# Performance work log

Hardware: AMD Instinct MI355X
Metric: run time of the kernel (lower is better)

## Reference

```python
import jax, jax.numpy as jnp
import numpy as np

N_NODES = 20000
N_EDGES = 50000
IN_DIM = 128
HID = 128
OUT_DIM = 64
N_PAIRS = 128
N_LAYERS = 2
N_HEADS = 4


def setup_inputs() -> dict:
    key = jax.random.key(0)
    ks = jax.random.split(key, 32)
    s = 0.05
    def p(k, shape):
        return jax.random.normal(k, shape, jnp.float32) * s
    inp = {}
    inp["node_features"] = jax.random.normal(ks[0], (N_NODES, IN_DIM), jnp.float32)
    inp["edge_index"] = jax.random.randint(ks[1], (2, N_EDGES), 0, N_NODES, jnp.int32)
    inp["edge_timestamps"] = jax.random.uniform(ks[2], (N_EDGES,), jnp.float32)
    inp["target_pairs"] = jax.random.randint(ks[3], (N_PAIRS, 2), 0, N_NODES, jnp.int32)
    inp["in_W"] = p(ks[4], (HID, IN_DIM)); inp["in_b"] = p(ks[5], (HID,))
    inp["te_W1"] = p(ks[6], (N_LAYERS, HID, 1)); inp["te_b1"] = p(ks[7], (N_LAYERS, HID))
    inp["te_W2"] = p(ks[8], (N_LAYERS, HID, HID)); inp["te_b2"] = p(ks[9], (N_LAYERS, HID))
    inp["attn_in_W"] = p(ks[10], (N_LAYERS, 3 * HID, HID)); inp["attn_in_b"] = p(ks[11], (N_LAYERS, 3 * HID))
    inp["attn_out_W"] = p(ks[12], (N_LAYERS, HID, HID)); inp["attn_out_b"] = p(ks[13], (N_LAYERS, HID))
    inp["ft_W"] = p(ks[14], (N_LAYERS, HID, HID)); inp["ft_b"] = p(ks[15], (N_LAYERS, HID))
    inp["op_W"] = p(ks[16], (N_LAYERS, HID, HID)); inp["op_b"] = p(ks[17], (N_LAYERS, HID))
    inp["out1_W"] = p(ks[18], (HID, HID)); inp["out1_b"] = p(ks[19], (HID,))
    inp["out2_W"] = p(ks[20], (OUT_DIM, HID)); inp["out2_b"] = p(ks[21], (OUT_DIM,))
    inp["lp1_W"] = p(ks[22], (HID, 2 * OUT_DIM)); inp["lp1_b"] = p(ks[23], (HID,))
    inp["lp2_W"] = p(ks[24], (HID // 2, HID)); inp["lp2_b"] = p(ks[25], (HID // 2,))
    inp["lp3_W"] = p(ks[26], (1, HID // 2)); inp["lp3_b"] = p(ks[27], (1,))
    return inp


def _forward(node_features, edge_index, edge_timestamps, target_pairs,
             in_W, in_b, te_W1, te_b1, te_W2, te_b2,
             attn_in_W, attn_in_b, attn_out_W, attn_out_b,
             ft_W, ft_b, op_W, op_b,
             out1_W, out1_b, out2_W, out2_b,
             lp1_W, lp1_b, lp2_W, lp2_b, lp3_W, lp3_b):
    N = node_features.shape[0]
    h = in_W.shape[0]
    H = N_HEADS
    d = h // H
    scale = 1.0 / np.sqrt(d).astype(np.float32)
    src, dst = edge_index[0], edge_index[1]
    # flattened target nodes; duplicates compute identical rows so dedup (torch.unique) is unneeded
    targets = target_pairs.reshape(-1)  # [U]
    U = targets.shape[0]
    E = src.shape[0]

    x = node_features @ in_W.T + in_b  # [N, h]
    for l in range(te_W1.shape[0]):
        tf = x @ ft_W[l].T + ft_b[l]                                           # [N, h]
        tfeat = jax.nn.relu(edge_timestamps[:, None] @ te_W1[l].T + te_b1[l])
        tfeat = tfeat @ te_W2[l].T + te_b2[l]                                  # [E, h]
        Wq, Wk, Wv = jnp.split(attn_in_W[l], 3, axis=0)
        bq, bk, bv = jnp.split(attn_in_b[l], 3)
        q = (tf[targets] @ Wq.T + bq).reshape(U, H, d)
        # keys/values are linear in (tf[nbr] + tfeat): split into node term A and edge term B
        Ak = (tf @ Wk.T).reshape(N, H, d)
        Bk = (tfeat @ Wk.T + bk).reshape(E, H, d)
        Av = (tf @ Wv.T).reshape(N, H, d)
        Bv = (tfeat @ Wv.T + bv).reshape(E, H, d)
        is_src = src[None, :] == targets[:, None]          # [U, E]
        mask = is_src | (dst[None, :] == targets[:, None])  # edge incident to target
        nbr = jnp.where(is_src, dst[None, :], src[None, :])  # other endpoint, [U, E]
        qAk = jnp.einsum('uhd,nhd->uhn', q, Ak) * scale      # [U, H, N]
        idx = jnp.broadcast_to(nbr[:, None, :], (U, H, E))
        s_node = jnp.take_along_axis(qAk, idx, axis=2)        # [U, H, E]
        s_edge = jnp.einsum('uhd,ehd->uhe', q, Bk) * scale
        scores = jnp.where(mask[:, None, :], s_node + s_edge, -1e30)
        p = jax.nn.softmax(scores, axis=-1)
        p = jnp.where(mask[:, None, :], p, 0.0)               # [U, H, E]
        out_edge = jnp.einsum('uhe,ehd->uhd', p, Bv)
        # sum_e p * Av[nbr] via per-target scatter of probs into node space
        w = jax.vmap(lambda pe, ne: jax.ops.segment_sum(pe, ne, num_segments=N))(
            p.transpose(0, 2, 1), nbr)                        # [U, N, H]
        out_node = jnp.einsum('unh,nhd->uhd', w, Av)
        attn = (out_node + out_edge).reshape(U, h) @ attn_out_W[l].T + attn_out_b[l]
        has_nbr = mask.any(axis=1)
        agg_in = jnp.where(has_nbr[:, None], attn, tf[targets])
        agg = agg_in @ op_W[l].T + op_b[l]
        x = x.at[targets].set(agg)
        x = jax.nn.relu(x)
    emb = jax.nn.relu(x @ out1_W.T + out1_b) @ out2_W.T + out2_b  # [N, out]
    pair = jnp.concatenate([emb[target_pairs[:, 0]], emb[target_pairs[:, 1]]], axis=1)
    z = jax.nn.relu(pair @ lp1_W.T + lp1_b)
    z = jax.nn.relu(z @ lp2_W.T + lp2_b)
    return jax.nn.sigmoid(z @ lp3_W.T + lp3_b)  # [B, 1]


def reference(node_features, edge_index, edge_timestamps, target_pairs,
              in_W, in_b, te_W1, te_b1, te_W2, te_b2,
              attn_in_W, attn_in_b, attn_out_W, attn_out_b,
              ft_W, ft_b, op_W, op_b,
              out1_W, out1_b, out2_W, out2_b,
              lp1_W, lp1_b, lp2_W, lp2_b, lp3_W, lp3_b):
    return _forward(node_features, edge_index, edge_timestamps, target_pairs,
                    in_W, in_b, te_W1, te_b1, te_W2, te_b2,
                    attn_in_W, attn_in_b, attn_out_W, attn_out_b,
                    ft_W, ft_b, op_W, op_b,
                    out1_W, out1_b, out2_W, out2_b,
                    lp1_W, lp1_b, lp2_W, lp2_b, lp3_W, lp3_b)
```

## Files before the change

kernel.cpp:

```cpp
#include <hip/hip_runtime.h>
#include <math.h>

#define N_NODES 20000
#define N_EDGES 50000
#define N_SLOTS 256
#define N_PAIRS 128
#define CAP 32
#define MSTRIDE 16384
#define NMAT 19
#define TFLAG (1 << 30)
#define HSZ 1024
#define NBLK 256
#define BATCH 16

__device__ __forceinline__ float4 relu4(float4 v) {
    return make_float4(fmaxf(v.x, 0.f), fmaxf(v.y, 0.f), fmaxf(v.z, 0.f), fmaxf(v.w, 0.f));
}
__device__ __forceinline__ float4 add4(float4 a, float4 b) {
    return make_float4(a.x + b.x, a.y + b.y, a.z + b.z, a.w + b.w);
}
__device__ __forceinline__ void fma4(float4& acc, const float4 w, const float s) {
    acc.x = fmaf(w.x, s, acc.x); acc.y = fmaf(w.y, s, acc.y);
    acc.z = fmaf(w.z, s, acc.z); acc.w = fmaf(w.w, s, acc.w);
}
#define F4Z make_float4(0.f, 0.f, 0.f, 0.f)

__device__ __forceinline__ void gbar(unsigned* cnt, unsigned target, bool wait) {
    __syncthreads();
    if (threadIdx.x == 0) {
        __builtin_amdgcn_fence(__ATOMIC_RELEASE, "agent");
        __hip_atomic_fetch_add(cnt, 1u, __ATOMIC_RELAXED, __HIP_MEMORY_SCOPE_AGENT);
        if (wait) {
            int it = 0;
            while (true) {
                unsigned v;
                if ((it++ & 7) != 7)
                    v = __hip_atomic_load(cnt, __ATOMIC_RELAXED,
                                          __HIP_MEMORY_SCOPE_SYSTEM);
                else
                    v = __hip_atomic_fetch_add(cnt, 0u, __ATOMIC_RELAXED,
                                               __HIP_MEMORY_SCOPE_AGENT);
                if (v >= target) break;
                __builtin_amdgcn_s_sleep(16);
            }
            __builtin_amdgcn_fence(__ATOMIC_ACQUIRE, "agent");
        }
    }
    __syncthreads();
}

__device__ __forceinline__ float4 mv_ks1_g8(const float* __restrict__ WT,
                                            const float* __restrict__ xv128,
                                            int g, int jj) {
    const float4* W4 = (const float4*)WT;
    const float4* x4 = (const float4*)xv128;
    float4 acc = F4Z;
#pragma unroll
    for (int kk4 = 0; kk4 < 4; ++kk4) {
        int k4 = g * 4 + kk4;
        float4 xv = x4[k4];
        fma4(acc, W4[(k4 * 4 + 0) * 32 + jj], xv.x);
        fma4(acc, W4[(k4 * 4 + 1) * 32 + jj], xv.y);
        fma4(acc, W4[(k4 * 4 + 2) * 32 + jj], xv.z);
        fma4(acc, W4[(k4 * 4 + 3) * 32 + jj], xv.w);
    }
    return acc;
}
__device__ __forceinline__ float4 mv_ks1_g8_64(const float* __restrict__ WT,
                                               const float* __restrict__ xv128,
                                               int g, int jj) {
    const float4* W4 = (const float4*)WT;
    const float4* x4 = (const float4*)xv128;
    int j16 = jj & 15;
    float4 acc = F4Z;
#pragma unroll
    for (int kk4 = 0; kk4 < 4; ++kk4) {
        int k4 = g * 4 + kk4;
        float4 xv = x4[k4];
        fma4(acc, W4[(k4 * 4 + 0) * 16 + j16], xv.x);
        fma4(acc, W4[(k4 * 4 + 1) * 16 + j16], xv.y);
        fma4(acc, W4[(k4 * 4 + 2) * 16 + j16], xv.z);
        fma4(acc, W4[(k4 * 4 + 3) * 16 + j16], xv.w);
    }
    return acc;
}
__device__ __forceinline__ float4 comb1_g8(const float4* pb, int jj) {
    float4 s = pb[jj];
#pragma unroll
    for (int gp = 1; gp < 8; ++gp) s = add4(s, pb[gp * 32 + jj]);
    return s;
}

__device__ __forceinline__ void mv16_g8(const float* __restrict__ WT,
                                        const float* __restrict__ xs,
                                        int g, int jj, float4* acc) {
    const float4* W4 = (const float4*)WT;
    const float4* x4 = (const float4*)xs;
#pragma unroll
    for (int kk4 = 0; kk4 < 4; ++kk4) {
        int k4 = g * 4 + kk4;
        float4 w0 = W4[(k4 * 4 + 0) * 32 + jj];
        float4 w1 = W4[(k4 * 4 + 1) * 32 + jj];
        float4 w2 = W4[(k4 * 4 + 2) * 32 + jj];
        float4 w3 = W4[(k4 * 4 + 3) * 32 + jj];
#pragma unroll
        for (int e = 0; e < 16; ++e) {
            float4 xv = x4[e * 32 + k4];
            fma4(acc[e], w0, xv.x); fma4(acc[e], w1, xv.y);
            fma4(acc[e], w2, xv.z); fma4(acc[e], w3, xv.w);
        }
    }
}
__device__ __forceinline__ float4 comb16_g8(const float4* pb, int it, int jj) {
    float4 s = pb[it * 32 + jj];
#pragma unroll
    for (int gp = 1; gp < 8; ++gp) s = add4(s, pb[(gp * 16 + it) * 32 + jj]);
    return s;
}

__device__ __forceinline__ float4 mv_ks1(const float* __restrict__ WT,
                                         const float* __restrict__ xv128,
                                         int g, int jj) {
    const float4* W4 = (const float4*)WT;
    const float4* x4 = (const float4*)xv128;
    float4 acc = F4Z;
#pragma unroll 2
    for (int kk4 = 0; kk4 < 8; ++kk4) {
        int k4 = g * 8 + kk4;
        float4 xv = x4[k4];
        fma4(acc, W4[(k4 * 4 + 0) * 32 + jj], xv.x);
        fma4(acc, W4[(k4 * 4 + 1) * 32 + jj], xv.y);
        fma4(acc, W4[(k4 * 4 + 2) * 32 + jj], xv.z);
        fma4(acc, W4[(k4 * 4 + 3) * 32 + jj], xv.w);
    }
    return acc;
}
__device__ __forceinline__ float4 mv_ks1_64(const float* __restrict__ WT,
                                            const float* __restrict__ xv128,
                                            int g, int jj) {
    const float4* W4 = (const float4*)WT;
    const float4* x4 = (const float4*)xv128;
    int j16 = jj & 15;
    float4 acc = F4Z;
#pragma unroll 2
    for (int kk4 = 0; kk4 < 8; ++kk4) {
        int k4 = g * 8 + kk4;
        float4 xv = x4[k4];
        fma4(acc, W4[(k4 * 4 + 0) * 16 + j16], xv.x);
        fma4(acc, W4[(k4 * 4 + 1) * 16 + j16], xv.y);
        fma4(acc, W4[(k4 * 4 + 2) * 16 + j16], xv.z);
        fma4(acc, W4[(k4 * 4 + 3) * 16 + j16], xv.w);
    }
    return acc;
}
__device__ __forceinline__ float4 comb1(const float4* pb, int jj) {
    return add4(add4(pb[jj], pb[32 + jj]), add4(pb[64 + jj], pb[96 + jj]));
}

__device__ __forceinline__ unsigned thash(int key) {
    return ((unsigned)key * 2654435761u) >> 22;
}
__device__ __forceinline__ bool hexists(const int* __restrict__ hkey, int key) {
    unsigned h = thash(key);
    while (true) {
        int k = hkey[h];
        if (k == -1) return false;
        if (k == key) return true;
        h = (h + 1) & (HSZ - 1);
    }
}
__device__ __forceinline__ void hemit_g(const int* __restrict__ hkey,
                                        const int* __restrict__ hval,
                                        int* __restrict__ gcnt,
                                        int2* __restrict__ lst,
                                        int key, int e, int nbrf) {
    unsigned h = thash(key);
    while (true) {
        int k = hkey[h];
        if (k == -1) return;
        if (k == key) {
            int s = hval[h];
            int pos = atomicAdd(&gcnt[s], 1);
            if (pos < CAP) lst[s * CAP + pos] = make_int2(e, nbrf);
        }
        h = (h + 1) & (HSZ - 1);
    }
}

struct Params {
    const float* nf; const int* ei; const float* ts; const int* tp;
    const float* inW; const float* inb;
    const float* teW1; const float* teb1; const float* teW2; const float* teb2;
    const float* aiW; const float* aib; const float* aoW; const float* aob;
    const float* ftW; const float* ftb; const float* opW; const float* opb;
    const float* o1W; const float* o1b; const float* o2W; const float* o2b;
    const float* l1W; const float* l1b; const float* l2W; const float* l2b;
    const float* l3W; const float* l3b;
    float* out; float* x; int* cnt; int2* lst; float* emb; float* WT;
    unsigned* bar;
};

__global__ __launch_bounds__(256, 1) void k_fused(Params P) {
    __shared__ __align__(16) float xu[128], x0u[128], tfv[128], qv[128], sv[128];
    __shared__ __align__(16) float xs[BATCH * 128], t1s[BATCH * 128];
    __shared__ __align__(16) float x0s[BATCH * 128], zs[BATCH * 128];
    __shared__ __align__(16) float4 pb[8 * 16 * 32];
    __shared__ __align__(16) float vbl[CAP * 128];
    __shared__ float scl[CAP * 4];
    __shared__ int nbr_s[BATCH], tf_s[BATCH];
    __shared__ float ts_s[BATCH];
    __shared__ __align__(16) float tile[32][129];
    __shared__ int hkey[HSZ], hval[HSZ];

    const int b = blockIdx.x, tid = threadIdx.x, g = tid >> 5, jj = tid & 31;

    if (b < 72) {
        int m, r0, rows;
        if (b < 68) { m = b >> 2; r0 = (b & 3) * 32; rows = 128; }
        else { int mm = b - 68; m = 17 + (mm >> 1); r0 = (mm & 1) * 32; rows = 64; }
        const float* src;
        if (m == 0) src = P.inW;
        else if (m <= 2) src = P.ftW + (m - 1) * MSTRIDE;
        else if (m <= 4) src = P.teW2 + (m - 3) * MSTRIDE;
        else if (m <= 10) src = P.aiW + (m - 5) * MSTRIDE;
        else if (m <= 12) src = P.aoW + (m - 11) * MSTRIDE;
        else if (m <= 14) src = P.opW + (m - 13) * MSTRIDE;
        else if (m == 15) src = P.o1W;
        else if (m == 16) src = P.l1W;
        else if (m == 17) src = P.o2W;
        else src = P.l2W;
        float* dst = P.WT + m * MSTRIDE;
        for (int idx = tid; idx < 32 * 128; idx += 256) {
            int r = idx >> 7, cc = idx & 127;
            tile[r][cc] = src[(r0 + r) * 128 + cc];
        }
        __syncthreads();
        for (int idx = tid; idx < 128 * 32; idx += 256) {
            int k = idx >> 5, jr = idx & 31;
            dst[k * rows + r0 + jr] = tile[jr][k];
        }
    } else {
        for (int i = tid; i < HSZ; i += 256) hkey[i] = -1;
        __syncthreads();
        {
            int uu = P.tp[tid];
            unsigned h = thash(uu);
            while (atomicCAS(&hkey[h], -1, uu) != -1) h = (h + 1) & (HSZ - 1);
            hval[h] = tid;
        }
        __syncthreads();
        const int4* s4 = (const int4*)P.ei;
        const int4* d4 = (const int4*)(P.ei + N_EDGES);
        const int NE4 = N_EDGES / 4;
        const int nscan = NBLK - 72;
        const int chunk = (NE4 + nscan - 1) / nscan;
        const int start = (b - 72) * chunk;
        const int end = min(start + chunk, NE4);
        for (int e4 = start + tid; e4 < end; e4 += 256) {
            int4 s = s4[e4];
            int4 d = d4[e4];
            int ss[4] = {s.x, s.y, s.z, s.w};
            int dd[4] = {d.x, d.y, d.z, d.w};
#pragma unroll
            for (int t = 0; t < 4; ++t) {
                int a = ss[t], bb = dd[t];
                bool atgt = hexists(hkey, a);
                bool btgt = (bb == a) ? atgt : hexists(hkey, bb);
                if (!atgt && !btgt) continue;
                int e = e4 * 4 + t;
                if (atgt) hemit_g(hkey, hval, P.cnt, P.lst, a, e, bb | (btgt ? TFLAG : 0));
                if (btgt && bb != a) hemit_g(hkey, hval, P.cnt, P.lst, bb, e, a | (atgt ? TFLAG : 0));
            }
        }
    }
    gbar(P.bar, NBLK, true);

    const float scale = 0.17677669529663687f;
    const int u = P.tp[b];
    const int c = min(P.cnt[b], CAP);

    for (int layer = 0; layer < 2; ++layer) {
        const float* WT_in = P.WT;
        const float* WT_ft = P.WT + (1 + layer) * MSTRIDE;
        const float* WT_te2 = P.WT + (3 + layer) * MSTRIDE;
        const float* WT_q = P.WT + (5 + 3 * layer) * MSTRIDE;
        const float* WT_k = P.WT + (6 + 3 * layer) * MSTRIDE;
        const float* WT_v = P.WT + (7 + 3 * layer) * MSTRIDE;
        const float* WT_ao = P.WT + (11 + layer) * MSTRIDE;
        const float* WT_op = P.WT + (13 + layer) * MSTRIDE;
        const float* inb = P.inb;
        const float* ftb = P.ftb + layer * 128;
        const float* teW1 = P.teW1 + layer * 128;
        const float* teb1 = P.teb1 + layer * 128;
        const float* teb2 = P.teb2 + layer * 128;
        const float* bq = P.aib + layer * 384;
        const float* bk = bq + 128;
        const float* bv = bq + 256;
        const float* aob = P.aob + layer * 128;
        const float* opb = P.opb + layer * 128;

        if (tid < 128) xu[tid] = (layer == 0) ? P.nf[(size_t)u * 128 + tid]
                                              : P.x[(size_t)u * 128 + tid];
        __syncthreads();
        const float* xeff = xu;
        if (layer == 0) {
            pb[g * 32 + jj] = mv_ks1_g8(WT_in, xu, g, jj);
            __syncthreads();
            if (g == 0)
                *(float4*)(x0u + jj * 4) = add4(comb1_g8(pb, jj), *(const float4*)(inb + jj * 4));
            xeff = x0u;
            __syncthreads();
        }
        pb[g * 32 + jj] = mv_ks1_g8(WT_ft, xeff, g, jj);
        __syncthreads();
        if (g == 0)
            *(float4*)(tfv + jj * 4) = add4(comb1_g8(pb, jj), *(const float4*)(ftb + jj * 4));
        __syncthreads();
        pb[g * 32 + jj] = mv_ks1_g8(WT_q, tfv, g, jj);
        __syncthreads();
        if (g == 0)
            *(float4*)(qv + jj * 4) = add4(comb1_g8(pb, jj), *(const float4*)(bq + jj * 4));
        __syncthreads();

        for (int base = 0; base < c; base += BATCH) {
            if (tid < BATCH) {
                int i = base + tid;
                int2 en = (i < c) ? P.lst[b * CAP + i] : make_int2(0, 0);
                nbr_s[tid] = en.y & ~TFLAG;
                tf_s[tid] = (en.y & TFLAG) ? 1 : 0;
                ts_s[tid] = (i < c) ? P.ts[en.x] : 0.f;
            }
            __syncthreads();
            {
                int c0 = jj * 4;
                float4 w = *(const float4*)(teW1 + c0);
                float4 bb = *(const float4*)(teb1 + c0);
#pragma unroll
                for (int s = 0; s < 2; ++s) {
                    int e = g + s * 8;
                    const float* srcp = (layer == 0) ? (P.nf + (size_t)nbr_s[e] * 128 + c0)
                                                     : (P.x + (size_t)nbr_s[e] * 128 + c0);
                    float4 v = *(const float4*)srcp;
                    float* dstp = (layer == 0) ? xs : x0s;
                    *(float4*)(dstp + e * 128 + c0) = v;
                    float tse = ts_s[e];
                    *(float4*)(t1s + e * 128 + c0) =
                        make_float4(fmaxf(fmaf(tse, w.x, bb.x), 0.f),
                                    fmaxf(fmaf(tse, w.y, bb.y), 0.f),
                                    fmaxf(fmaf(tse, w.z, bb.z), 0.f),
                                    fmaxf(fmaf(tse, w.w, bb.w), 0.f));
                }
            }
            __syncthreads();
            if (layer == 0) {
                float4 acc[16] = {F4Z, F4Z, F4Z, F4Z, F4Z, F4Z, F4Z, F4Z,
                                  F4Z, F4Z, F4Z, F4Z, F4Z, F4Z, F4Z, F4Z};
                mv16_g8(WT_in, xs, g, jj, acc);
#pragma unroll
                for (int e = 0; e < 16; ++e) pb[(g * 16 + e) * 32 + jj] = acc[e];
                __syncthreads();
#pragma unroll
                for (int s = 0; s < 2; ++s) {
                    int it = 2 * g + s;
                    float4 x0v = add4(comb16_g8(pb, it, jj), *(const float4*)(inb + jj * 4));
                    *(float4*)(x0s + it * 128 + jj * 4) = x0v;
                    if (base + it < c && !tf_s[it])
                        *(float4*)(P.x + (size_t)nbr_s[it] * 128 + jj * 4) = relu4(x0v);
                }
                __syncthreads();
            }
            {
                float4 acc[16] = {F4Z, F4Z, F4Z, F4Z, F4Z, F4Z, F4Z, F4Z,
                                  F4Z, F4Z, F4Z, F4Z, F4Z, F4Z, F4Z, F4Z};
                mv16_g8(WT_ft, x0s, g, jj, acc);
                mv16_g8(WT_te2, t1s, g, jj, acc);
#pragma unroll
                for (int e = 0; e < 16; ++e) pb[(g * 16 + e) * 32 + jj] = acc[e];
                __syncthreads();
                float4 zb4 = add4(*(const float4*)(ftb + jj * 4),
                                  *(const float4*)(teb2 + jj * 4));
#pragma unroll
                for (int s = 0; s < 2; ++s) {
                    int it = 2 * g + s;
                    *(float4*)(zs + it * 128 + jj * 4) = add4(comb16_g8(pb, it, jj), zb4);
                }
                __syncthreads();
            }
            {
                float4 acc[16] = {F4Z, F4Z, F4Z, F4Z, F4Z, F4Z, F4Z, F4Z,
                                  F4Z, F4Z, F4Z, F4Z, F4Z, F4Z, F4Z, F4Z};
                mv16_g8(WT_k, zs, g, jj, acc);
#pragma unroll
                for (int e = 0; e < 16; ++e) pb[(g * 16 + e) * 32 + jj] = acc[e];
                __syncthreads();
                float4 q4 = *(const float4*)(qv + jj * 4);
#pragma unroll
                for (int s = 0; s < 2; ++s) {
                    int it = 2 * g + s;
                    float4 kk = add4(comb16_g8(pb, it, jj), *(const float4*)(bk + jj * 4));
                    float pr = q4.x * kk.x + q4.y * kk.y + q4.z * kk.z + q4.w * kk.w;
                    pr += __shfl_xor(pr, 1);
                    pr += __shfl_xor(pr, 2);
                    pr += __shfl_xor(pr, 4);
                    if (base + it < c && (jj & 7) == 0)
                        scl[(base + it) * 4 + (jj >> 3)] = pr * scale;
                }
                __syncthreads();
            }
            {
                float4 acc[16] = {F4Z, F4Z, F4Z, F4Z, F4Z, F4Z, F4Z, F4Z,
                                  F4Z, F4Z, F4Z, F4Z, F4Z, F4Z, F4Z, F4Z};
                mv16_g8(WT_v, zs, g, jj, acc);
#pragma unroll
                for (int e = 0; e < 16; ++e) pb[(g * 16 + e) * 32 + jj] = acc[e];
                __syncthreads();
#pragma unroll
                for (int s = 0; s < 2; ++s) {
                    int it = 2 * g + s;
                    float4 vv = add4(comb16_g8(pb, it, jj), *(const float4*)(bv + jj * 4));
                    if (base + it < c)
                        *(float4*)(vbl + (base + it) * 128 + jj * 4) = vv;
                }
                __syncthreads();
            }
        }

        if (tid < 128) {
            int hd = tid >> 5;
            if (c > 0) {
                float m = -INFINITY;
                for (int i = 0; i < c; ++i) m = fmaxf(m, scl[i * 4 + hd]);
                float l = 0.f, o = 0.f;
                for (int i = 0; i < c; ++i) {
                    float p = __expf(scl[i * 4 + hd] - m);
                    l += p;
                    o = fmaf(p, vbl[i * 128 + tid], o);
                }
                sv[tid] = o / l;
            } else {
                sv[tid] = 0.f;
            }
        }
        __syncthreads();
        pb[g * 32 + jj] = mv_ks1_g8(WT_ao, sv, g, jj);
        __syncthreads();
        if (g == 0) {
            float4 z4;
            if (c > 0) z4 = add4(comb1_g8(pb, jj), *(const float4*)(aob + jj * 4));
            else z4 = *(const float4*)(tfv + jj * 4);
            *(float4*)(xu + jj * 4) = z4;
        }
        __syncthreads();
        pb[g * 32 + jj] = mv_ks1_g8(WT_op, xu, g, jj);
        __syncthreads();
        if (layer == 0) {
            if (g == 0) {
                float4 a = relu4(add4(comb1_g8(pb, jj), *(const float4*)(opb + jj * 4)));
                *(float4*)(P.x + (size_t)u * 128 + jj * 4) = a;
            }
        } else {
            if (g == 0)
                *(float4*)(x0u + jj * 4) =
                    relu4(add4(comb1_g8(pb, jj), *(const float4*)(opb + jj * 4)));
            __syncthreads();
            pb[g * 32 + jj] = mv_ks1_g8(P.WT + 15 * MSTRIDE, x0u, g, jj);
            __syncthreads();
            if (g == 0)
                *(float4*)(tfv + jj * 4) =
                    relu4(add4(comb1_g8(pb, jj), *(const float4*)(P.o1b + jj * 4)));
            __syncthreads();
            pb[g * 32 + jj] = mv_ks1_g8_64(P.WT + 17 * MSTRIDE, tfv, g, jj);
            __syncthreads();
            if (g == 0 && jj < 16)
                *(float4*)(P.emb + (size_t)b * 64 + jj * 4) =
                    add4(comb1_g8(pb, jj), *(const float4*)(P.o2b + jj * 4));
        }
        gbar(P.bar, NBLK * (2 + layer), layer == 0 || b < N_PAIRS);
    }

    if (b < N_PAIRS) {
        const float* WT_l1 = P.WT + 16 * MSTRIDE;
        const float* WT_l2 = P.WT + 18 * MSTRIDE;
        if (tid < 128)
            xu[tid] = (tid < 64) ? P.emb[(size_t)(2 * b) * 64 + tid]
                                 : P.emb[(size_t)(2 * b + 1) * 64 + (tid - 64)];
        __syncthreads();
        if (tid < 128) pb[g * 32 + jj] = mv_ks1(WT_l1, xu, g, jj);
        __syncthreads();
        if (tid < 128 && g == 0)
            *(float4*)(tfv + jj * 4) =
                relu4(add4(comb1(pb, jj), *(const float4*)(P.l1b + jj * 4)));
        __syncthreads();
        if (tid < 128) pb[g * 32 + jj] = mv_ks1_64(WT_l2, tfv, g, jj);
        __syncthreads();
        if (tid < 128 && g == 0 && jj < 16)
            *(float4*)(qv + jj * 4) =
                relu4(add4(comb1(pb, jj), *(const float4*)(P.l2b + jj * 4)));
        __syncthreads();
        if (tid < 64) {
            float v = qv[tid] * P.l3W[tid];
            v += __shfl_xor(v, 1);
            v += __shfl_xor(v, 2);
            v += __shfl_xor(v, 4);
            v += __shfl_xor(v, 8);
            v += __shfl_xor(v, 16);
            v += __shfl_xor(v, 32);
            if (tid == 0) P.out[b] = 1.f / (1.f + __expf(-(v + P.l3b[0])));
        }
    }
}

extern "C" void kernel_launch(void* const* d_in, const int* in_sizes, int n_in,
                              void* d_out, int out_size, void* d_ws, size_t ws_size,
                              hipStream_t stream) {
    Params P;
    P.nf  = (const float*)d_in[0];
    P.ei  = (const int*)d_in[1];
    P.ts  = (const float*)d_in[2];
    P.tp  = (const int*)d_in[3];
    P.inW = (const float*)d_in[4];
    P.inb = (const float*)d_in[5];
    P.teW1 = (const float*)d_in[6];
    P.teb1 = (const float*)d_in[7];
    P.teW2 = (const float*)d_in[8];
    P.teb2 = (const float*)d_in[9];
    P.aiW = (const float*)d_in[10];
    P.aib = (const float*)d_in[11];
    P.aoW = (const float*)d_in[12];
    P.aob = (const float*)d_in[13];
    P.ftW = (const float*)d_in[14];
    P.ftb = (const float*)d_in[15];
    P.opW = (const float*)d_in[16];
    P.opb = (const float*)d_in[17];
    P.o1W = (const float*)d_in[18];
    P.o1b = (const float*)d_in[19];
    P.o2W = (const float*)d_in[20];
    P.o2b = (const float*)d_in[21];
    P.l1W = (const float*)d_in[22];
    P.l1b = (const float*)d_in[23];
    P.l2W = (const float*)d_in[24];
    P.l2b = (const float*)d_in[25];
    P.l3W = (const float*)d_in[26];
    P.l3b = (const float*)d_in[27];
    P.out = (float*)d_out;

    char* ws = (char*)d_ws;
    size_t off = 0;
    P.x    = (float*)(ws + off); off += (size_t)N_NODES * 128 * 4;
    P.cnt  = (int*)  (ws + off); off += N_SLOTS * 4;
    P.lst  = (int2*) (ws + off); off += (size_t)N_SLOTS * CAP * 8;
    P.emb  = (float*)(ws + off); off += N_SLOTS * 64 * 4;
    P.WT   = (float*)(ws + off); off += (size_t)NMAT * MSTRIDE * 4;
    P.bar  = (unsigned*)(ws + off); off += 256;

    hipMemsetAsync(P.cnt, 0, N_SLOTS * 4, stream);
    hipMemsetAsync(P.bar, 0, 4, stream);
    k_fused<<<NBLK, 256, 0, stream>>>(P);
}
```

Baseline: 196.5 us.

## Keep matvec chain in registers with wave-level combine and ping-pong buffers

Replaces the per-step pattern (partial sums to shared, wave 0 combines, writes a shared vector, barrier, all waves reread) with a combine done in every wave via xor-shuffles. Each wave reduces exactly the input chunk it needs for the next matvec and keeps it in registers. Alternating two partial-sum buffers removes one __syncthreads per matvec in the serial chain of dependent 128x128 matvecs. The cost is redundant reduction work in every wave and more register use.

```diff
diff --git a/kernel.cpp b/kernel.cpp
--- a/kernel.cpp
+++ b/kernel.cpp
@@ -24,6 +24,14 @@
     acc.z = fmaf(w.z, s, acc.z); acc.w = fmaf(w.w, s, acc.w);
 }
 #define F4Z make_float4(0.f, 0.f, 0.f, 0.f)
+__device__ __forceinline__ float4 shfl4(float4 v, int src) {
+    return make_float4(__shfl(v.x, src, 32), __shfl(v.y, src, 32),
+                       __shfl(v.z, src, 32), __shfl(v.w, src, 32));
+}
+__device__ __forceinline__ float4 xorsum4(float4 v, int m) {
+    return make_float4(v.x + __shfl_xor(v.x, m), v.y + __shfl_xor(v.y, m),
+                       v.z + __shfl_xor(v.z, m), v.w + __shfl_xor(v.w, m));
+}
 
 __device__ __forceinline__ void gbar(unsigned* cnt, unsigned target, bool wait) {
     __syncthreads();
@@ -49,40 +57,50 @@
     __syncthreads();
 }
 
-__device__ __forceinline__ float4 mv_ks1_g8(const float* __restrict__ WT,
-                                            const float* __restrict__ xv128,
-                                            int g, int jj) {
+__device__ __forceinline__ float4 mv_reg_g8(const float* __restrict__ WT,
+                                            const float4 xv[4], int g, int jj) {
     const float4* W4 = (const float4*)WT;
-    const float4* x4 = (const float4*)xv128;
     float4 acc = F4Z;
 #pragma unroll
     for (int kk4 = 0; kk4 < 4; ++kk4) {
         int k4 = g * 4 + kk4;
-        float4 xv = x4[k4];
-        fma4(acc, W4[(k4 * 4 + 0) * 32 + jj], xv.x);
-        fma4(acc, W4[(k4 * 4 + 1) * 32 + jj], xv.y);
-        fma4(acc, W4[(k4 * 4 + 2) * 32 + jj], xv.z);
-        fma4(acc, W4[(k4 * 4 + 3) * 32 + jj], xv.w);
+        float4 x = xv[kk4];
+        fma4(acc, W4[(k4 * 4 + 0) * 32 + jj], x.x);
+        fma4(acc, W4[(k4 * 4 + 1) * 32 + jj], x.y);
+        fma4(acc, W4[(k4 * 4 + 2) * 32 + jj], x.z);
+        fma4(acc, W4[(k4 * 4 + 3) * 32 + jj], x.w);
     }
     return acc;
 }
-__device__ __forceinline__ float4 mv_ks1_g8_64(const float* __restrict__ WT,
-                                               const float* __restrict__ xv128,
-                                               int g, int jj) {
+__device__ __forceinline__ float4 mv_reg_g8_64(const float* __restrict__ WT,
+                                               const float4 xv[4], int g, int jj) {
     const float4* W4 = (const float4*)WT;
-    const float4* x4 = (const float4*)xv128;
     int j16 = jj & 15;
     float4 acc = F4Z;
 #pragma unroll
     for (int kk4 = 0; kk4 < 4; ++kk4) {
         int k4 = g * 4 + kk4;
-        float4 xv = x4[k4];
-        fma4(acc, W4[(k4 * 4 + 0) * 16 + j16], xv.x);
-        fma4(acc, W4[(k4 * 4 + 1) * 16 + j16], xv.y);
-        fma4(acc, W4[(k4 * 4 + 2) * 16 + j16], xv.z);
-        fma4(acc, W4[(k4 * 4 + 3) * 16 + j16], xv.w);
+        float4 x = xv[kk4];
+        fma4(acc, W4[(k4 * 4 + 0) * 16 + j16], x.x);
+        fma4(acc, W4[(k4 * 4 + 1) * 16 + j16], x.y);
+        fma4(acc, W4[(k4 * 4 + 2) * 16 + j16], x.z);
+        fma4(acc, W4[(k4 * 4 + 3) * 16 + j16], x.w);
     }
     return acc;
+}
+__device__ __forceinline__ void comb_wave(const float4* pbuf, int g, int jj,
+                                          const float* __restrict__ bias,
+                                          float4 xv[4]) {
+    int col = jj >> 3, gp = jj & 7;
+    float4 v = pbuf[gp * 32 + g * 4 + col];
+    v = xorsum4(v, 1); v = xorsum4(v, 2); v = xorsum4(v, 4);
+    v = add4(v, *(const float4*)(bias + (g * 4 + col) * 4));
+#pragma unroll
+    for (int cc = 0; cc < 4; ++cc) xv[cc] = shfl4(v, cc * 8);
+}
+__device__ __forceinline__ void store_chunk(float* dst, int g, int jj,
+                                            const float4 xv[4]) {
+    if ((jj & 7) == 0) *(float4*)(dst + (g * 4 + (jj >> 3)) * 4) = xv[jj >> 3];
 }
 __device__ __forceinline__ float4 comb1_g8(const float4* pb, int jj) {
     float4 s = pb[jj];
@@ -201,7 +219,7 @@
 };
 
 __global__ __launch_bounds__(256, 1) void k_fused(Params P) {
-    __shared__ __align__(16) float xu[128], x0u[128], tfv[128], qv[128], sv[128];
+    __shared__ __align__(16) float xu[128], tfv[128], qv[128], sv[128];
     __shared__ __align__(16) float xs[BATCH * 128], t1s[BATCH * 128];
     __shared__ __align__(16) float x0s[BATCH * 128], zs[BATCH * 128];
     __shared__ __align__(16) float4 pb[8 * 16 * 32];
@@ -213,6 +231,8 @@
     __shared__ int hkey[HSZ], hval[HSZ];
 
     const int b = blockIdx.x, tid = threadIdx.x, g = tid >> 5, jj = tid & 31;
+    float4* pbA = pb;
+    float4* pbB = pb + 32 * 32;
 
     if (b < 72) {
         int m, r0, rows;
@@ -299,28 +319,31 @@
         const float* aob = P.aob + layer * 128;
         const float* opb = P.opb + layer * 128;
 
-        if (tid < 128) xu[tid] = (layer == 0) ? P.nf[(size_t)u * 128 + tid]
-                                              : P.x[(size_t)u * 128 + tid];
-        __syncthreads();
-        const float* xeff = xu;
+        float4 xva[4];
+        {
+            const float* xsrc = (layer == 0) ? (P.nf + (size_t)u * 128)
+                                             : (P.x + (size_t)u * 128);
+#pragma unroll
+            for (int cc = 0; cc < 4; ++cc)
+                xva[cc] = *(const float4*)(xsrc + (g * 4 + cc) * 4);
+        }
         if (layer == 0) {
-            pb[g * 32 + jj] = mv_ks1_g8(WT_in, xu, g, jj);
+            pbA[g * 32 + jj] = mv_reg_g8(WT_in, xva, g, jj);
             __syncthreads();
-            if (g == 0)
-                *(float4*)(x0u + jj * 4) = add4(comb1_g8(pb, jj), *(const float4*)(inb + jj * 4));
-            xeff = x0u;
-            __syncthreads();
-        }
-        pb[g * 32 + jj] = mv_ks1_g8(WT_ft, xeff, g, jj);
-        __syncthreads();
-        if (g == 0)
-            *(float4*)(tfv + jj * 4) = add4(comb1_g8(pb, jj), *(const float4*)(ftb + jj * 4));
-        __syncthreads();
-        pb[g * 32 + jj] = mv_ks1_g8(WT_q, tfv, g, jj);
-        __syncthreads();
-        if (g == 0)
-            *(float4*)(qv + jj * 4) = add4(comb1_g8(pb, jj), *(const float4*)(bq + jj * 4));
-        __syncthreads();
+            comb_wave(pbA, g, jj, inb, xva);
+        }
+        pbB[g * 32 + jj] = mv_reg_g8(WT_ft, xva, g, jj);
+        __syncthreads();
+        float4 xvt[4];
+        comb_wave(pbB, g, jj, ftb, xvt);
+        store_chunk(tfv, g, jj, xvt);
+        pbA[g * 32 + jj] = mv_reg_g8(WT_q, xvt, g, jj);
+        __syncthreads();
+        {
+            float4 xvq[4];
+            comb_wave(pbA, g, jj, bq, xvq);
+            store_chunk(qv, g, jj, xvq);
+        }
 
         for (int base = 0; base < c; base += BATCH) {
             if (tid < BATCH) {
@@ -442,38 +465,40 @@
             }
         }
         __syncthreads();
-        pb[g * 32 + jj] = mv_ks1_g8(WT_ao, sv, g, jj);
-        __syncthreads();
-        if (g == 0) {
-            float4 z4;
-            if (c > 0) z4 = add4(comb1_g8(pb, jj), *(const float4*)(aob + jj * 4));
-            else z4 = *(const float4*)(tfv + jj * 4);
-            *(float4*)(xu + jj * 4) = z4;
-        }
-        __syncthreads();
-        pb[g * 32 + jj] = mv_ks1_g8(WT_op, xu, g, jj);
-        __syncthreads();
+        float4 xvz[4];
+        {
+            float4 xvs[4];
+#pragma unroll
+            for (int cc = 0; cc < 4; ++cc)
+                xvs[cc] = *(const float4*)(sv + (g * 4 + cc) * 4);
+            pbA[g * 32 + jj] = mv_reg_g8(WT_ao, xvs, g, jj);
+        }
+        __syncthreads();
+        comb_wave(pbA, g, jj, aob, xvz);
+        if (c == 0) {
+#pragma unroll
+            for (int cc = 0; cc < 4; ++cc)
+                xvz[cc] = *(const float4*)(tfv + (g * 4 + cc) * 4);
+        }
+        pbB[g * 32 + jj] = mv_reg_g8(WT_op, xvz, g, jj);
+        __syncthreads();
+        comb_wave(pbB, g, jj, opb, xvz);
+#pragma unroll
+        for (int cc = 0; cc < 4; ++cc) xvz[cc] = relu4(xvz[cc]);
         if (layer == 0) {
-            if (g == 0) {
-                float4 a = relu4(add4(comb1_g8(pb, jj), *(const float4*)(opb + jj * 4)));
-                *(float4*)(P.x + (size_t)u * 128 + jj * 4) = a;
-            }
+            if ((jj & 7) == 0)
+                *(float4*)(P.x + (size_t)u * 128 + (g * 4 + (jj >> 3)) * 4) = xvz[jj >> 3];
         } else {
-            if (g == 0)
-                *(float4*)(x0u + jj * 4) =
-                    relu4(add4(comb1_g8(pb, jj), *(const float4*)(opb + jj * 4)));
+            pbA[g * 32 + jj] = mv_reg_g8(P.WT + 15 * MSTRIDE, xvz, g, jj);
             __syncthreads();
-            pb[g * 32 + jj] = mv_ks1_g8(P.WT + 15 * MSTRIDE, x0u, g, jj);
-            __syncthreads();
-            if (g == 0)
-                *(float4*)(tfv + jj * 4) =
-                    relu4(add4(comb1_g8(pb, jj), *(const float4*)(P.o1b + jj * 4)));
-            __syncthreads();
-            pb[g * 32 + jj] = mv_ks1_g8_64(P.WT + 17 * MSTRIDE, tfv, g, jj);
+            comb_wave(pbA, g, jj, P.o1b, xvz);
+#pragma unroll
+            for (int cc = 0; cc < 4; ++cc) xvz[cc] = relu4(xvz[cc]);
+            pbB[g * 32 + jj] = mv_reg_g8_64(P.WT + 17 * MSTRIDE, xvz, g, jj);
             __syncthreads();
             if (g == 0 && jj < 16)
                 *(float4*)(P.emb + (size_t)b * 64 + jj * 4) =
-                    add4(comb1_g8(pb, jj), *(const float4*)(P.o2b + jj * 4));
+                    add4(comb1_g8(pbB, jj), *(const float4*)(P.o2b + jj * 4));
         }
         gbar(P.bar, NBLK * (2 + layer), layer == 0 || b < N_PAIRS);
     }
```

New measurement: 206.2 us. 1.05x slower.

## Fold query into K weights and apply V projection after softmax aggregation

Applied to the files above, without the earlier changes.

Removes the per-neighbor K and V matrix-vector products. Scores are computed as z·(Wk^T q_h) + q·bk using a per-head folded vector built once per layer. V is applied once per head to the softmax-weighted sum of z, which works because the softmax weights sum to one. This cuts the dense matvec work per batch from three to one, at the cost of storing all z rows in shared memory (CAP×128) and adding a small fold step per layer.

```diff
diff --git a/kernel.cpp b/kernel.cpp
--- a/kernel.cpp
+++ b/kernel.cpp
@@ -203,10 +203,12 @@
 __global__ __launch_bounds__(256, 1) void k_fused(Params P) {
     __shared__ __align__(16) float xu[128], x0u[128], tfv[128], qv[128], sv[128];
     __shared__ __align__(16) float xs[BATCH * 128], t1s[BATCH * 128];
-    __shared__ __align__(16) float x0s[BATCH * 128], zs[BATCH * 128];
+    __shared__ __align__(16) float x0s[BATCH * 128];
+    __shared__ __align__(16) float zs[CAP * 128];
     __shared__ __align__(16) float4 pb[8 * 16 * 32];
-    __shared__ __align__(16) float vbl[CAP * 128];
-    __shared__ float scl[CAP * 4];
+    __shared__ __align__(16) float qkh[4 * 128];
+    __shared__ __align__(16) float zbl[4 * 128];
+    __shared__ float scl[CAP * 4], ps[CAP * 4], sbk[4];
     __shared__ int nbr_s[BATCH], tf_s[BATCH];
     __shared__ float ts_s[BATCH];
     __shared__ __align__(16) float tile[32][129];
@@ -284,7 +286,6 @@
         const float* WT_ft = P.WT + (1 + layer) * MSTRIDE;
         const float* WT_te2 = P.WT + (3 + layer) * MSTRIDE;
         const float* WT_q = P.WT + (5 + 3 * layer) * MSTRIDE;
-        const float* WT_k = P.WT + (6 + 3 * layer) * MSTRIDE;
         const float* WT_v = P.WT + (7 + 3 * layer) * MSTRIDE;
         const float* WT_ao = P.WT + (11 + layer) * MSTRIDE;
         const float* WT_op = P.WT + (13 + layer) * MSTRIDE;
@@ -320,6 +321,27 @@
         __syncthreads();
         if (g == 0)
             *(float4*)(qv + jj * 4) = add4(comb1_g8(pb, jj), *(const float4*)(bq + jj * 4));
+        __syncthreads();
+        {
+            const float* WkRaw = P.aiW + (size_t)layer * 3 * MSTRIDE + MSTRIDE;
+            int i = tid & 127, hb = tid >> 7;
+#pragma unroll
+            for (int s = 0; s < 2; ++s) {
+                int h = hb * 2 + s;
+                float a = 0.f;
+#pragma unroll 8
+                for (int j = 0; j < 32; ++j)
+                    a = fmaf(WkRaw[(size_t)(h * 32 + j) * 128 + i], qv[h * 32 + j], a);
+                qkh[h * 128 + i] = a;
+            }
+            if (tid < 128) {
+                float pp = qv[tid] * bk[tid];
+                pp += __shfl_xor(pp, 1, 32); pp += __shfl_xor(pp, 2, 32);
+                pp += __shfl_xor(pp, 4, 32); pp += __shfl_xor(pp, 8, 32);
+                pp += __shfl_xor(pp, 16, 32);
+                if ((tid & 31) == 0) sbk[tid >> 5] = pp;
+            }
+        }
         __syncthreads();
 
         for (int base = 0; base < c; base += BATCH) {
@@ -382,64 +404,69 @@
 #pragma unroll
                 for (int s = 0; s < 2; ++s) {
                     int it = 2 * g + s;
-                    *(float4*)(zs + it * 128 + jj * 4) = add4(comb16_g8(pb, it, jj), zb4);
+                    *(float4*)(zs + (size_t)(base + it) * 128 + jj * 4) =
+                        add4(comb16_g8(pb, it, jj), zb4);
                 }
                 __syncthreads();
             }
             {
-                float4 acc[16] = {F4Z, F4Z, F4Z, F4Z, F4Z, F4Z, F4Z, F4Z,
-                                  F4Z, F4Z, F4Z, F4Z, F4Z, F4Z, F4Z, F4Z};
-                mv16_g8(WT_k, zs, g, jj, acc);
-#pragma unroll
-                for (int e = 0; e < 16; ++e) pb[(g * 16 + e) * 32 + jj] = acc[e];
-                __syncthreads();
-                float4 q4 = *(const float4*)(qv + jj * 4);
-#pragma unroll
-                for (int s = 0; s < 2; ++s) {
-                    int it = 2 * g + s;
-                    float4 kk = add4(comb16_g8(pb, it, jj), *(const float4*)(bk + jj * 4));
-                    float pr = q4.x * kk.x + q4.y * kk.y + q4.z * kk.z + q4.w * kk.w;
-                    pr += __shfl_xor(pr, 1);
-                    pr += __shfl_xor(pr, 2);
-                    pr += __shfl_xor(pr, 4);
-                    if (base + it < c && (jj & 7) == 0)
-                        scl[(base + it) * 4 + (jj >> 3)] = pr * scale;
+                int it = tid >> 4, l = tid & 15, item = base + it;
+                const float* zp = zs + (size_t)item * 128;
+                float s0 = 0.f, s1 = 0.f, s2 = 0.f, s3 = 0.f;
+#pragma unroll
+                for (int dd = 0; dd < 8; ++dd) {
+                    int d = dd * 16 + l;
+                    float zv = zp[d];
+                    s0 = fmaf(qkh[d], zv, s0);
+                    s1 = fmaf(qkh[128 + d], zv, s1);
+                    s2 = fmaf(qkh[256 + d], zv, s2);
+                    s3 = fmaf(qkh[384 + d], zv, s3);
+                }
+                s0 += __shfl_xor(s0, 1, 16); s0 += __shfl_xor(s0, 2, 16);
+                s0 += __shfl_xor(s0, 4, 16); s0 += __shfl_xor(s0, 8, 16);
+                s1 += __shfl_xor(s1, 1, 16); s1 += __shfl_xor(s1, 2, 16);
+                s1 += __shfl_xor(s1, 4, 16); s1 += __shfl_xor(s1, 8, 16);
+                s2 += __shfl_xor(s2, 1, 16); s2 += __shfl_xor(s2, 2, 16);
+                s2 += __shfl_xor(s2, 4, 16); s2 += __shfl_xor(s2, 8, 16);
+                s3 += __shfl_xor(s3, 1, 16); s3 += __shfl_xor(s3, 2, 16);
+                s3 += __shfl_xor(s3, 4, 16); s3 += __shfl_xor(s3, 8, 16);
+                if (l == 0 && item < c) {
+                    scl[item * 4 + 0] = (s0 + sbk[0]) * scale;
+                    scl[item * 4 + 1] = (s1 + sbk[1]) * scale;
+                    scl[item * 4 + 2] = (s2 + sbk[2]) * scale;
+                    scl[item * 4 + 3] = (s3 + sbk[3]) * scale;
                 }
                 __syncthreads();
             }
-            {
-                float4 acc[16] = {F4Z, F4Z, F4Z, F4Z, F4Z, F4Z, F4Z, F4Z,
-                                  F4Z, F4Z, F4Z, F4Z, F4Z, F4Z, F4Z, F4Z};
-                mv16_g8(WT_v, zs, g, jj, acc);
-#pragma unroll
-                for (int e = 0; e < 16; ++e) pb[(g * 16 + e) * 32 + jj] = acc[e];
-                __syncthreads();
-#pragma unroll
-                for (int s = 0; s < 2; ++s) {
-                    int it = 2 * g + s;
-                    float4 vv = add4(comb16_g8(pb, it, jj), *(const float4*)(bv + jj * 4));
-                    if (base + it < c)
-                        *(float4*)(vbl + (base + it) * 128 + jj * 4) = vv;
-                }
-                __syncthreads();
-            }
-        }
-
-        if (tid < 128) {
-            int hd = tid >> 5;
-            if (c > 0) {
-                float m = -INFINITY;
-                for (int i = 0; i < c; ++i) m = fmaxf(m, scl[i * 4 + hd]);
-                float l = 0.f, o = 0.f;
-                for (int i = 0; i < c; ++i) {
-                    float p = __expf(scl[i * 4 + hd] - m);
-                    l += p;
-                    o = fmaf(p, vbl[i * 128 + tid], o);
-                }
-                sv[tid] = o / l;
-            } else {
-                sv[tid] = 0.f;
-            }
+        }
+
+        if (tid < 128 && c > 0) {
+            int hd = tid >> 5, e = tid & 31;
+            float m = -INFINITY;
+            for (int i = 0; i < c; ++i) m = fmaxf(m, scl[i * 4 + hd]);
+            float l = 0.f;
+            for (int i = 0; i < c; ++i) l += __expf(scl[i * 4 + hd] - m);
+            if (e < c) ps[e * 4 + hd] = __expf(scl[e * 4 + hd] - m) / l;
+        }
+        __syncthreads();
+        {
+            int i = tid & 127, hb = tid >> 7;
+#pragma unroll
+            for (int s = 0; s < 2; ++s) {
+                int h = hb * 2 + s;
+                float a = 0.f;
+                for (int e = 0; e < c; ++e)
+                    a = fmaf(ps[e * 4 + h], zs[(size_t)e * 128 + i], a);
+                zbl[h * 128 + i] = a;
+            }
+        }
+        __syncthreads();
+        pb[g * 32 + jj] = mv_ks1_g8(WT_v, zbl + (jj >> 3) * 128, g, jj);
+        __syncthreads();
+        if (g == 0) {
+            float4 vv = add4(comb1_g8(pb, jj), *(const float4*)(bv + jj * 4));
+            if (c == 0) vv = F4Z;
+            *(float4*)(sv + jj * 4) = vv;
         }
         __syncthreads();
         pb[g * 32 + jj] = mv_ks1_g8(WT_ao, sv, g, jj);
```

New measurement: 196.2 us (median of 2 runs). About the same (-0.1%).
